# Optimization experiments

Measured on AMD Instinct MI355X. Metric: run time of the kernel, lower is better.

Reference implementation:

```python
import jax, jax.numpy as jnp
import numpy as np

N, D, C = 131072, 512, 1000

def setup_inputs() -> dict:
    key = jax.random.key(0)
    k1, k2, k3 = jax.random.split(key, 3)
    features = jax.random.normal(k1, (N, D), dtype=jnp.float32)
    labels = jax.random.randint(k2, (N,), 0, C, dtype=jnp.int64)
    prototypes = jax.random.normal(k3, (C, D), dtype=jnp.float32)
    return {"features": features, "labels": labels, "prototypes": prototypes}

def reference(features, labels, prototypes):
    # Original: for each sample, squared euclidean distance to the prototype of
    # its label (prototypes indexed by position of label in sorted unique labels;
    # with all C classes present, that is prototypes[label]), then mean over N.
    # Returned with shape (1, 1) to match the torch module's accumulated dists.
    gathered = prototypes[labels]                      # [N, D] gather by label
    sq = (features - gathered) ** 2                    # fused diff+square
    per_sample = jnp.sum(sq, axis=1)                   # [N]
    loss = jnp.mean(per_sample)
    return loss.reshape(1, 1)
```

## Files before the change

### kernel.cpp

```cpp
#include <hip/hip_runtime.h>


constexpr int N_ROWS = 131072;
constexpr int DIM    = 512;
constexpr int D4     = DIM / 4;
constexpr int BLOCK  = 256;
constexpr int GRID   = 2048;

__global__ void zero_out_kernel(float* out) { out[0] = 0.0f; }

__global__ __launch_bounds__(BLOCK) void proto_loss_kernel(
    const float4* __restrict__ features,
    const int*    __restrict__ labels,
    const float4* __restrict__ prototypes,
    float* __restrict__ out)
{
    const long long total  = (long long)N_ROWS * D4;
    const long long stride = (long long)GRID * BLOCK;
    long long idx = (long long)blockIdx.x * BLOCK + threadIdx.x;

    float acc = 0.0f;
    for (; idx < total; idx += stride) {
        const int row = (int)(idx >> 7);
        const int c4  = (int)(idx & (D4 - 1));
        const int lab = labels[row];
        const float4 f = features[idx];
        const float4 p = prototypes[lab * D4 + c4];
        const float dx = f.x - p.x;
        const float dy = f.y - p.y;
        const float dz = f.z - p.z;
        const float dw = f.w - p.w;
        acc += dx * dx + dy * dy + dz * dz + dw * dw;
    }

    #pragma unroll
    for (int off = 32; off > 0; off >>= 1)
        acc += __shfl_down(acc, off, 64);

    __shared__ float wave_sums[BLOCK / 64];
    const int lane = threadIdx.x & 63;
    const int wid  = threadIdx.x >> 6;
    if (lane == 0) wave_sums[wid] = acc;
    __syncthreads();

    if (threadIdx.x == 0) {
        float s = 0.0f;
        #pragma unroll
        for (int w = 0; w < BLOCK / 64; ++w) s += wave_sums[w];
        atomicAdd(out, s * (1.0f / (float)N_ROWS));
    }
}

extern "C" void kernel_launch(void* const* d_in, const int* in_sizes, int n_in,
                              void* d_out, int out_size, void* d_ws, size_t ws_size,
                              hipStream_t stream) {
    const float4* features   = (const float4*)d_in[0];
    const int*    labels     = (const int*)d_in[1];
    const float4* prototypes = (const float4*)d_in[2];
    float* out = (float*)d_out;

    zero_out_kernel<<<1, 1, 0, stream>>>(out);
    proto_loss_kernel<<<GRID, BLOCK, 0, stream>>>(features, labels, prototypes, out);
}
```

Before: 370.7 us.

## Assign contiguous rows per wave with nontemporal feature loads and two-pass reduction

Each wavefront now handles a contiguous block of 16 rows. The row index and label come from a wave-uniform scalar, so the per-element label gather and index math go away. Feature loads use nontemporal hints so the streaming 256MB input does not evict the prototype table from cache. The atomic accumulation and zero kernel are replaced by per-block partials in workspace plus a single-block reduce kernel. The cost is an extra launch and the assumption that the row count divides evenly across waves.

```diff
diff --git a/kernel.cpp b/kernel.cpp
--- a/kernel.cpp
+++ b/kernel.cpp
@@ -1,36 +1,42 @@
 #include <hip/hip_runtime.h>
 
 
+typedef float fvec4 __attribute__((ext_vector_type(4)));
+
 constexpr int N_ROWS = 131072;
-constexpr int DIM    = 512;
-constexpr int D4     = DIM / 4;
+constexpr int D4     = 128;
 constexpr int BLOCK  = 256;
 constexpr int GRID   = 2048;
+constexpr int WAVES  = GRID * (BLOCK / 64);
+constexpr int ROWS_PER_WAVE = N_ROWS / WAVES;
 
-__global__ void zero_out_kernel(float* out) { out[0] = 0.0f; }
-
-__global__ __launch_bounds__(BLOCK) void proto_loss_kernel(
-    const float4* __restrict__ features,
-    const int*    __restrict__ labels,
-    const float4* __restrict__ prototypes,
-    float* __restrict__ out)
+__global__ __launch_bounds__(BLOCK) void proto_loss_main(
+    const fvec4* __restrict__ features,
+    const int*   __restrict__ labels,
+    const fvec4* __restrict__ prototypes,
+    float* __restrict__ partials)
 {
-    const long long total  = (long long)N_ROWS * D4;
-    const long long stride = (long long)GRID * BLOCK;
-    long long idx = (long long)blockIdx.x * BLOCK + threadIdx.x;
+    const int lane = threadIdx.x & 63;
+    const int wid  = threadIdx.x >> 6;
+    const int wave = __builtin_amdgcn_readfirstlane(blockIdx.x * (BLOCK / 64) + wid);
+    const int row0 = wave * ROWS_PER_WAVE;
 
     float acc = 0.0f;
-    for (; idx < total; idx += stride) {
-        const int row = (int)(idx >> 7);
-        const int c4  = (int)(idx & (D4 - 1));
+    #pragma unroll 4
+    for (int i = 0; i < ROWS_PER_WAVE; ++i) {
+        const int row = row0 + i;
         const int lab = labels[row];
-        const float4 f = features[idx];
-        const float4 p = prototypes[lab * D4 + c4];
-        const float dx = f.x - p.x;
-        const float dy = f.y - p.y;
-        const float dz = f.z - p.z;
-        const float dw = f.w - p.w;
-        acc += dx * dx + dy * dy + dz * dz + dw * dw;
+        const long long fbase = (long long)row * D4;
+        const fvec4 f0 = __builtin_nontemporal_load(features + fbase + lane);
+        const fvec4 f1 = __builtin_nontemporal_load(features + fbase + 64 + lane);
+        const fvec4* prow = prototypes + lab * D4;
+        const fvec4 p0 = prow[lane];
+        const fvec4 p1 = prow[lane + 64];
+
+        fvec4 d0 = f0 - p0;
+        fvec4 d1 = f1 - p1;
+        acc += d0.x * d0.x + d0.y * d0.y + d0.z * d0.z + d0.w * d0.w
+             + d1.x * d1.x + d1.y * d1.y + d1.z * d1.z + d1.w * d1.w;
     }
 
     #pragma unroll
@@ -38,8 +44,6 @@
         acc += __shfl_down(acc, off, 64);
 
     __shared__ float wave_sums[BLOCK / 64];
-    const int lane = threadIdx.x & 63;
-    const int wid  = threadIdx.x >> 6;
     if (lane == 0) wave_sums[wid] = acc;
     __syncthreads();
 
@@ -47,18 +51,44 @@
         float s = 0.0f;
         #pragma unroll
         for (int w = 0; w < BLOCK / 64; ++w) s += wave_sums[w];
-        atomicAdd(out, s * (1.0f / (float)N_ROWS));
+        partials[blockIdx.x] = s;
+    }
+}
+
+__global__ __launch_bounds__(BLOCK) void proto_loss_reduce(
+    const float* __restrict__ partials, float* __restrict__ out)
+{
+    float s = 0.0f;
+    for (int i = threadIdx.x; i < GRID; i += BLOCK)
+        s += partials[i];
+
+    #pragma unroll
+    for (int off = 32; off > 0; off >>= 1)
+        s += __shfl_down(s, off, 64);
+
+    __shared__ float wave_sums[BLOCK / 64];
+    const int lane = threadIdx.x & 63;
+    const int wid  = threadIdx.x >> 6;
+    if (lane == 0) wave_sums[wid] = s;
+    __syncthreads();
+
+    if (threadIdx.x == 0) {
+        float t = 0.0f;
+        #pragma unroll
+        for (int w = 0; w < BLOCK / 64; ++w) t += wave_sums[w];
+        out[0] = t * (1.0f / (float)N_ROWS);
     }
 }
 
 extern "C" void kernel_launch(void* const* d_in, const int* in_sizes, int n_in,
                               void* d_out, int out_size, void* d_ws, size_t ws_size,
                               hipStream_t stream) {
-    const float4* features   = (const float4*)d_in[0];
-    const int*    labels     = (const int*)d_in[1];
-    const float4* prototypes = (const float4*)d_in[2];
-    float* out = (float*)d_out;
+    const fvec4* features   = (const fvec4*)d_in[0];
+    const int*   labels     = (const int*)d_in[1];
+    const fvec4* prototypes = (const fvec4*)d_in[2];
+    float* partials = (float*)d_ws;
+    float* out      = (float*)d_out;
 
-    zero_out_kernel<<<1, 1, 0, stream>>>(out);
-    proto_loss_kernel<<<GRID, BLOCK, 0, stream>>>(features, labels, prototypes, out);
+    proto_loss_main<<<GRID, BLOCK, 0, stream>>>(features, labels, prototypes, partials);
+    proto_loss_reduce<<<1, BLOCK, 0, stream>>>(partials, out);
 }
```

New measurement: 339.7 us, median of 2. 8.4% less time.
